# Kernel optimization log

Hardware: AMD Instinct MI355X
Metric: run time of the kernel (lower is better)

Reference implementation:

```python
import jax, jax.numpy as jnp
import numpy as np

INF = 1000000000.0
D = 1024


def setup_inputs() -> dict:
    key = jax.random.key(0)
    k_enc, k_r = jax.random.split(key)
    encoding = jax.random.normal(k_enc, (8, 2048, D), dtype=jnp.float32)
    R = jax.random.normal(k_r, (D, D), dtype=jnp.float32) / D  # init_with_zeros=False
    return {"encoding": encoding, "R": R}


def reference(encoding, R):
    b, n, d = encoding.shape
    # Q = encoding @ R ; scores = Q @ encoding^T  (bilinear relation attention)
    encR = jnp.einsum("bnd,de->bne", encoding, R)          # [b, n, d]
    scores = jnp.einsum("bnd,bmd->bnm", encR, encoding)     # [b, n, n]
    # causal mask: -INF above the diagonal (use_mask=True)
    mask = jnp.where(jnp.tril(jnp.ones((n, n), dtype=bool)), 0.0, -INF).astype(scores.dtype)
    A = jax.nn.softmax(scores + mask, axis=2)               # [b, n, n]
    return jnp.einsum("bnm,bmd->bnd", A, encoding)          # [b, n, d]
```

## Files before the change

kernel.cpp:

```cpp
#include <hip/hip_runtime.h>
#include <hip/hip_bf16.h>


typedef __attribute__((ext_vector_type(4))) float f32x4;
typedef __attribute__((ext_vector_type(4))) unsigned u32x4;
typedef __attribute__((ext_vector_type(8))) __fp16 f16x8;
typedef __attribute__((ext_vector_type(4))) __fp16 f16x4;
typedef __attribute__((ext_vector_type(2))) __fp16 f16x2;

#define MFMA16H(A, B, C) __builtin_amdgcn_mfma_f32_16x16x32_f16(A, B, C, 0, 0, 0)

__device__ __forceinline__ f16x4 cvt4h(f32x4 a) {
    union { f16x4 v; f16x2 h[2]; } r;
    r.h[0] = __builtin_amdgcn_cvt_pkrtz(a[0], a[1]);
    r.h[1] = __builtin_amdgcn_cvt_pkrtz(a[2], a[3]);
    return r.v;
}

__device__ __forceinline__ void gload16(const void* g, void* l) {
    __builtin_amdgcn_global_load_lds(
        (const __attribute__((address_space(1))) unsigned*)g,
        (__attribute__((address_space(3))) unsigned*)l, 16, 0, 0);
}

#define BAR() do { __builtin_amdgcn_sched_barrier(0); \
                   __builtin_amdgcn_s_barrier();      \
                   __builtin_amdgcn_sched_barrier(0); } while (0)

__global__ __launch_bounds__(256) void transpose_cvt_kernel(
    const float* __restrict__ enc, __fp16* __restrict__ encT, __fp16* __restrict__ encH,
    const float* __restrict__ R, __fp16* __restrict__ Rt)
{
    __shared__ __align__(16) char lt[64 * 128];
    const int t = threadIdx.x;
    const int bz = blockIdx.z;
    const bool isR = (bz == 8);
    if (isR && blockIdx.x >= 16) return;
    const int Rr = isR ? 1024 : 2048, C = 1024;
    const float* src = isR ? R : enc;
    __fp16* dstT = isR ? Rt : encT;
    __fp16* dstH = isR ? (__fp16*)nullptr : encH;
    const int r0 = blockIdx.x * 64, c0 = blockIdx.y * 64;
    const size_t so = isR ? 0 : (size_t)bz * Rr * C;
    const int tr = t >> 4;
    const int tc4 = (t & 15) * 4;
#pragma unroll
    for (int p = 0; p < 4; ++p) {
        int rl = tr + 16 * p;
        f32x4 x = *(const f32x4*)(src + so + (size_t)(r0 + rl) * C + c0 + tc4);
        f16x4 h = cvt4h(x);
        if (dstH) *(f16x4*)(dstH + so + (size_t)(r0 + rl) * C + c0 + tc4) = h;
        *(f16x4*)(lt + rl * 128 + ((tc4 * 2) ^ ((rl & 7) << 4))) = h;
    }
    __syncthreads();
#pragma unroll
    for (int p = 0; p < 4; ++p) {
        int dl = tr + 16 * p;
#pragma unroll
        for (int j = 0; j < 4; ++j) {
            int kl = (t & 15) + 16 * j;
            __fp16 v = *(const __fp16*)(lt + kl * 128 + ((dl * 2) ^ ((kl & 7) << 4)));
            dstT[so + (size_t)(c0 + dl) * Rr + r0 + kl] = v;
        }
    }
}

__global__ __launch_bounds__(512, 2) void gemm_qr256(
    const __fp16* __restrict__ encH, const __fp16* __restrict__ Rt,
    __fp16* __restrict__ Qh)
{
    __shared__ __align__(16) char lds[131072];
    const int t = threadIdx.x;
    const int w = t >> 6, l = t & 63;
    const int l15 = l & 15, lg = (l >> 4) & 3;
    const int wr = w >> 2, wc = w & 3;
    const int bm = ((int)blockIdx.x >> 2) * 256;
    const int bn = ((int)blockIdx.x & 3) * 256;
    const __fp16* Ag = encH + (size_t)bm * 1024;
    const __fp16* Bg = Rt + (size_t)bn * 1024;

    const int srow = 32 * w + (l >> 2);
    const int slg = ((l & 3) - ((l >> 3) & 3)) & 3;
    const int slotr = ((l >> 4) + ((l & 15) >> 1)) & 3;

    f32x4 acc[8][4];
#pragma unroll
    for (int i = 0; i < 8; ++i)
#pragma unroll
        for (int j = 0; j < 4; ++j) acc[i][j] = (f32x4){0.f, 0.f, 0.f, 0.f};

    auto stage = [&](int op, int tile, int kh) {
        const __fp16* src = (op ? Bg : Ag) + (size_t)srow * 1024 + tile * 64 + kh * 32 + slg * 8;
        char* dst = lds + (tile & 1) * 65536 + op * 32768 + kh * 16384 + w * 2048;
        gload16(src, dst);
        gload16(src + (size_t)16 * 1024, dst + 1024);
    };
    auto rdA = [&](int buf, int ks, int mf) {
        return *(const f16x8*)(lds + buf * 65536 + ks * 16384
                               + (128 * wr + 16 * mf + l15) * 64 + slotr * 16);
    };
    auto rdB = [&](int buf, int ks, int nf) {
        return *(const f16x8*)(lds + buf * 65536 + 32768 + ks * 16384
                               + (64 * wc + 16 * nf + l15) * 64 + slotr * 16);
    };

    stage(0, 0, 0); stage(1, 0, 0); stage(0, 0, 1); stage(1, 0, 1);
    stage(0, 1, 0); stage(1, 1, 0);

    f16x8 afr[4], bfr[4];

#define MF16(mbase)                                                     \
    __builtin_amdgcn_s_setprio(1);                                      \
    _Pragma("unroll") for (int mf = 0; mf < 4; ++mf)                    \
        _Pragma("unroll") for (int nf = 0; nf < 4; ++nf)                \
            acc[(mbase) + mf][nf] = MFMA16H(afr[mf], bfr[nf], acc[(mbase) + mf][nf]); \
    __builtin_amdgcn_s_setprio(0);

    for (int i = 0; i < 8; ++i) {
        const bool lastI = (i == 7);
        asm volatile("s_waitcnt vmcnt(8)" ::: "memory");
        BAR();
#pragma unroll
        for (int nf = 0; nf < 4; ++nf) bfr[nf] = rdB(0, 0, nf);
#pragma unroll
        for (int mf = 0; mf < 4; ++mf) afr[mf] = rdA(0, 0, mf);
        stage(0, 2 * i + 1, 1);
        MF16(0)
        BAR();
#pragma unroll
        for (int mf = 0; mf < 4; ++mf) afr[mf] = rdA(0, 0, mf + 4);
        stage(1, 2 * i + 1, 1);
        MF16(4)
        asm volatile("s_waitcnt vmcnt(8)" ::: "memory");
        BAR();
#pragma unroll
        for (int nf = 0; nf < 4; ++nf) bfr[nf] = rdB(0, 1, nf);
#pragma unroll
        for (int mf = 0; mf < 4; ++mf) afr[mf] = rdA(0, 1, mf);
        if (!lastI) stage(0, 2 * i + 2, 0);
        MF16(0)
        BAR();
#pragma unroll
        for (int mf = 0; mf < 4; ++mf) afr[mf] = rdA(0, 1, mf + 4);
        if (!lastI) stage(1, 2 * i + 2, 0);
        MF16(4)
        if (!lastI) asm volatile("s_waitcnt vmcnt(8)" ::: "memory");
        else        asm volatile("s_waitcnt vmcnt(4)" ::: "memory");
        BAR();
#pragma unroll
        for (int nf = 0; nf < 4; ++nf) bfr[nf] = rdB(1, 0, nf);
#pragma unroll
        for (int mf = 0; mf < 4; ++mf) afr[mf] = rdA(1, 0, mf);
        if (!lastI) stage(0, 2 * i + 2, 1);
        MF16(0)
        BAR();
#pragma unroll
        for (int mf = 0; mf < 4; ++mf) afr[mf] = rdA(1, 0, mf + 4);
        if (!lastI) stage(1, 2 * i + 2, 1);
        MF16(4)
        if (!lastI) asm volatile("s_waitcnt vmcnt(8)" ::: "memory");
        else        asm volatile("s_waitcnt vmcnt(0)" ::: "memory");
        BAR();
#pragma unroll
        for (int nf = 0; nf < 4; ++nf) bfr[nf] = rdB(1, 1, nf);
#pragma unroll
        for (int mf = 0; mf < 4; ++mf) afr[mf] = rdA(1, 1, mf);
        if (!lastI) stage(0, 2 * i + 3, 0);
        MF16(0)
        BAR();
#pragma unroll
        for (int mf = 0; mf < 4; ++mf) afr[mf] = rdA(1, 1, mf + 4);
        if (!lastI) stage(1, 2 * i + 3, 0);
        MF16(4)
    }
#undef MF16

#pragma unroll
    for (int mf = 0; mf < 8; ++mf)
#pragma unroll
        for (int nf = 0; nf < 4; ++nf)
#pragma unroll
            for (int rg = 0; rg < 4; ++rg) {
                int rr = bm + 128 * wr + 16 * mf + 4 * lg + rg;
                int cc = bn + 64 * wc + 16 * nf + l15;
                Qh[(size_t)rr * 1024 + cc] = (__fp16)acc[mf][nf][rg];
            }
}

template <int CMODE>
__device__ __forceinline__ void core256x128(
    const __fp16* __restrict__ A, int ldA, const __fp16* __restrict__ B, int ldB,
    char* __restrict__ Cptr, int ldC, int K, int rowOff, int colOff, bool maskDiag)
{
    __shared__ __align__(16) char lds[73728];
    const int t = threadIdx.x;
    const int w = t >> 6, l = t & 63;
    const int l15 = l & 15, lg = (l >> 4) & 3;
    const int wr = w >> 1, wc = w & 1;

    const int srowA = 32 * w + (l >> 2);
    const int srowB = 16 * w + (l >> 2);
    const int slg = ((l & 3) - ((l >> 3) & 3)) & 3;
    const int slotr = ((l >> 4) + ((l & 15) >> 1)) & 3;

    f32x4 acc[4][4];
#pragma unroll
    for (int i = 0; i < 4; ++i)
#pragma unroll
        for (int j = 0; j < 4; ++j) acc[i][j] = (f32x4){0.f, 0.f, 0.f, 0.f};

    auto stageH = [&](int h) {
        const int reg = h % 3;
        const __fp16* sa = A + (size_t)srowA * ldA + h * 32 + slg * 8;
        char* da = lds + reg * 16384 + w * 2048;
        gload16(sa, da);
        gload16(sa + (size_t)16 * ldA, da + 1024);
        const __fp16* sb = B + (size_t)srowB * ldB + h * 32 + slg * 8;
        gload16(sb, lds + 49152 + reg * 8192 + w * 1024);
    };
    auto rdA = [&](int h, int mf) {
        return *(const f16x8*)(lds + (h % 3) * 16384
                               + (64 * wr + 16 * mf + l15) * 64 + slotr * 16);
    };
    auto rdB = [&](int h, int nf) {
        return *(const f16x8*)(lds + 49152 + (h % 3) * 8192
                               + (64 * wc + 16 * nf + l15) * 64 + slotr * 16);
    };

    const int nh = K >> 5;
    stageH(0); stageH(1);

    f16x8 afr[4], bfr[4];
    for (int h = 0; h < nh; ++h) {
        if (h + 1 < nh) asm volatile("s_waitcnt vmcnt(3)" ::: "memory");
        else            asm volatile("s_waitcnt vmcnt(0)" ::: "memory");
        BAR();
#pragma unroll
        for (int nf = 0; nf < 4; ++nf) bfr[nf] = rdB(h, nf);
#pragma unroll
        for (int mf = 0; mf < 4; ++mf) afr[mf] = rdA(h, mf);
        if (h + 2 < nh) stageH(h + 2);
        __builtin_amdgcn_s_setprio(1);
#pragma unroll
        for (int mf = 0; mf < 4; ++mf)
#pragma unroll
            for (int nf = 0; nf < 4; ++nf)
                acc[mf][nf] = MFMA16H(afr[mf], bfr[nf], acc[mf][nf]);
        __builtin_amdgcn_s_setprio(0);
    }
    BAR();

#pragma unroll
    for (int mf = 0; mf < 4; ++mf)
#pragma unroll
        for (int nf = 0; nf < 4; ++nf)
#pragma unroll
            for (int rg = 0; rg < 4; ++rg) {
                int rr = 64 * wr + 16 * mf + 4 * lg + rg;
                int cc = 64 * wc + 16 * nf + l15;
                float v = acc[mf][nf][rg];
                if (CMODE == 2) {
                    *(float*)(Cptr + ((size_t)rr * ldC + cc) * 4) = v;
                } else {
                    if (maskDiag && colOff + cc > rowOff + rr) v = -30000.f;
                    *(__fp16*)(Cptr + ((size_t)rr * ldC + cc) * 2) = (__fp16)v;
                }
            }
}

__global__ __launch_bounds__(512, 4) void gemm_s256(
    const __fp16* __restrict__ Qh, const __fp16* __restrict__ encH,
    __fp16* __restrict__ S)
{
    const int b = (int)blockIdx.x & 7;
    const int r = (int)blockIdx.x >> 3;
    int qt = 0;
    while (r >= (qt + 1) * (qt + 2)) ++qt;
    const int nt = r - qt * (qt + 1);
    const size_t bo = (size_t)b * 2048 * 1024;
    const size_t so = (size_t)b * 2048 * 2048;
    core256x128<1>(Qh + bo + (size_t)(256 * qt) * 1024, 1024,
                   encH + bo + (size_t)(128 * nt) * 1024, 1024,
                   (char*)(S + so + (size_t)(256 * qt) * 2048 + 128 * nt), 2048,
                   1024, 256 * qt, 128 * nt, (nt >> 1) == qt);
}

__global__ __launch_bounds__(512, 4) void gemm_pv256(
    const __fp16* __restrict__ P, const __fp16* __restrict__ encT,
    float* __restrict__ out)
{
    const int b = (int)blockIdx.x & 7;
    const int r = (int)blockIdx.x >> 3;
    const int qtb = 7 - (r >> 3);
    const int dblk = r & 7;
    const size_t so = (size_t)b * 2048 * 2048;
    const size_t to = (size_t)b * 1024 * 2048;
    const size_t oo = (size_t)b * 2048 * 1024;
    core256x128<2>(P + so + (size_t)(256 * qtb) * 2048, 2048,
                   encT + to + (size_t)(128 * dblk) * 2048, 2048,
                   (char*)(out + oo + (size_t)(256 * qtb) * 1024 + 128 * dblk), 1024,
                   256 * (qtb + 1), 0, 0, false);
}

__global__ __launch_bounds__(256) void softmax_kernel(__fp16* __restrict__ S, int sh)
{
    const int t = threadIdx.x;
    const int wv = t >> 6, l = t & 63;
    const int r = blockIdx.x * 4 + wv;
    const int b = blockIdx.y;
    __fp16* row = S + ((size_t)b * 2048 + r) * 2048;
    const int L = ((r >> sh) + 1) << sh;

    float v[4][8];
    float mx = -1e30f;
#pragma unroll
    for (int i = 0; i < 4; ++i) {
        int c0 = 8 * l + 512 * i;
        if (c0 < L) {
            f16x8 h = *reinterpret_cast<const f16x8*>(row + c0);
#pragma unroll
            for (int j = 0; j < 8; ++j) { v[i][j] = (float)h[j]; mx = fmaxf(mx, v[i][j]); }
        } else {
#pragma unroll
            for (int j = 0; j < 8; ++j) v[i][j] = -1e30f;
        }
    }
#pragma unroll
    for (int off = 1; off < 64; off <<= 1) mx = fmaxf(mx, __shfl_xor(mx, off));
    float sm = 0.f;
#pragma unroll
    for (int i = 0; i < 4; ++i)
#pragma unroll
        for (int j = 0; j < 8; ++j) { v[i][j] = __expf(v[i][j] - mx); sm += v[i][j]; }
#pragma unroll
    for (int off = 1; off < 64; off <<= 1) sm += __shfl_xor(sm, off);
    const float inv = 1.f / sm;
#pragma unroll
    for (int i = 0; i < 4; ++i) {
        int c0 = 8 * l + 512 * i;
        if (c0 < L) {
            union { f16x8 v8; f16x2 h[4]; } o;
#pragma unroll
            for (int j = 0; j < 4; ++j)
                o.h[j] = __builtin_amdgcn_cvt_pkrtz(v[i][2 * j] * inv, v[i][2 * j + 1] * inv);
            *reinterpret_cast<f16x8*>(row + c0) = o.v8;
        }
    }
}

__global__ __launch_bounds__(256) void qr_gemm_kernel(
    const float* __restrict__ A, const float* __restrict__ B, float* C)
{
    __shared__ __align__(16) char sA[128 * 64];
    __shared__ __align__(16) char sB[128 * 64];
    const int t = threadIdx.x;
    const int w = t >> 6, l = t & 63;
    const int l15 = l & 15, lg = l >> 4;
    const int bm = blockIdx.x * 128;
    const int bn = blockIdx.y * 128;

    f32x4 acc[4][4];
#pragma unroll
    for (int i = 0; i < 4; ++i)
#pragma unroll
        for (int j = 0; j < 4; ++j) acc[i][j] = (f32x4){0.f, 0.f, 0.f, 0.f};

    const int kq = 4 * (t & 7);
    const int i2 = t >> 3;

    for (int kk = 0; kk < 1024; kk += 32) {
#pragma unroll
        for (int it = 0; it < 4; ++it) {
            int m = i2 + 32 * it;
            f32x4 x = *reinterpret_cast<const f32x4*>(&A[(size_t)(bm + m) * 1024 + kk + kq]);
            *reinterpret_cast<f16x4*>(sA + m * 64 + ((2 * kq) ^ (((m >> 1) & 3) << 4))) = cvt4h(x);
        }
        {
            int n0 = 4 * i2;
            f32x4 x[4];
#pragma unroll
            for (int r = 0; r < 4; ++r)
                x[r] = *reinterpret_cast<const f32x4*>(&B[(size_t)(kk + kq + r) * 1024 + bn + n0]);
#pragma unroll
            for (int j = 0; j < 4; ++j) {
                int n = n0 + j;
                union { f16x4 v; f16x2 h[2]; } s;
                s.h[0] = __builtin_amdgcn_cvt_pkrtz(x[0][j], x[1][j]);
                s.h[1] = __builtin_amdgcn_cvt_pkrtz(x[2][j], x[3][j]);
                *reinterpret_cast<f16x4*>(sB + n * 64 + ((2 * kq) ^ (((n >> 1) & 3) << 4))) = s.v;
            }
        }
        __syncthreads();
        f16x8 af[4], bfv[4];
        const int r0 = (w >> 1) * 64, c0 = (w & 1) * 64;
#pragma unroll
        for (int mt = 0; mt < 4; ++mt) {
            int m = r0 + 16 * mt + l15;
            af[mt] = *reinterpret_cast<f16x8*>(sA + m * 64 + ((16 * lg) ^ (((m >> 1) & 3) << 4)));
        }
#pragma unroll
        for (int nt = 0; nt < 4; ++nt) {
            int n = c0 + 16 * nt + l15;
            bfv[nt] = *reinterpret_cast<f16x8*>(sB + n * 64 + ((16 * lg) ^ (((n >> 1) & 3) << 4)));
        }
#pragma unroll
        for (int mt = 0; mt < 4; ++mt)
#pragma unroll
            for (int nt = 0; nt < 4; ++nt)
                acc[mt][nt] = MFMA16H(af[mt], bfv[nt], acc[mt][nt]);
        __syncthreads();
    }
#pragma unroll
    for (int mt = 0; mt < 4; ++mt)
#pragma unroll
        for (int nt = 0; nt < 4; ++nt)
#pragma unroll
            for (int rg = 0; rg < 4; ++rg) {
                int row = bm + (w >> 1) * 64 + 16 * mt + 4 * lg + rg;
                int col = bn + (w & 1) * 64 + 16 * nt + l15;
                C[(size_t)row * 1024 + col] = acc[mt][nt][rg];
            }
}

__global__ __launch_bounds__(256) void s_gemm_kernel(
    const float* __restrict__ Q, const float* __restrict__ enc, __fp16* __restrict__ S)
{
    __shared__ __align__(16) char sA[128 * 64];
    __shared__ __align__(16) char sB[128 * 64];
    const int t = threadIdx.x;
    const int w = t >> 6, l = t & 63;
    const int l15 = l & 15, lg = l >> 4;

    int rem = 135 - (int)blockIdx.x;
    int qt = 0;
    while (rem > qt) { rem -= qt + 1; ++qt; }
    const int kt = rem;
    const int b = blockIdx.y;
    const float* Arow = Q + ((size_t)b * 2048 + qt * 128) * 1024;
    const float* Brow = enc + ((size_t)b * 2048 + kt * 128) * 1024;

    f32x4 acc[4][4];
#pragma unroll
    for (int i = 0; i < 4; ++i)
#pragma unroll
        for (int j = 0; j < 4; ++j) acc[i][j] = (f32x4){0.f, 0.f, 0.f, 0.f};

    const int kq = 4 * (t & 7);
    const int i2 = t >> 3;

    for (int kk = 0; kk < 1024; kk += 32) {
#pragma unroll
        for (int it = 0; it < 4; ++it) {
            int m = i2 + 32 * it;
            int sw = (2 * kq) ^ (((m >> 1) & 3) << 4);
            f32x4 xa = *reinterpret_cast<const f32x4*>(&Arow[(size_t)m * 1024 + kk + kq]);
            f32x4 xb = *reinterpret_cast<const f32x4*>(&Brow[(size_t)m * 1024 + kk + kq]);
            *reinterpret_cast<f16x4*>(sA + m * 64 + sw) = cvt4h(xa);
            *reinterpret_cast<f16x4*>(sB + m * 64 + sw) = cvt4h(xb);
        }
        __syncthreads();
        f16x8 af[4], bfv[4];
        const int r0 = (w >> 1) * 64, c0 = (w & 1) * 64;
#pragma unroll
        for (int mt = 0; mt < 4; ++mt) {
            int m = r0 + 16 * mt + l15;
            af[mt] = *reinterpret_cast<f16x8*>(sA + m * 64 + ((16 * lg) ^ (((m >> 1) & 3) << 4)));
        }
#pragma unroll
        for (int nt = 0; nt < 4; ++nt) {
            int n = c0 + 16 * nt + l15;
            bfv[nt] = *reinterpret_cast<f16x8*>(sB + n * 64 + ((16 * lg) ^ (((n >> 1) & 3) << 4)));
        }
#pragma unroll
        for (int mt = 0; mt < 4; ++mt)
#pragma unroll
            for (int nt = 0; nt < 4; ++nt)
                acc[mt][nt] = MFMA16H(af[mt], bfv[nt], acc[mt][nt]);
        __syncthreads();
    }
    const int r0 = (w >> 1) * 64, c0 = (w & 1) * 64;
#pragma unroll
    for (int mt = 0; mt < 4; ++mt)
#pragma unroll
        for (int nt = 0; nt < 4; ++nt)
#pragma unroll
            for (int rg = 0; rg < 4; ++rg) {
                int rt = r0 + 16 * mt + 4 * lg + rg;
                int ct = c0 + 16 * nt + l15;
                float v = acc[mt][nt][rg];
                if (kt == qt && ct > rt) v = -30000.f;
                S[((size_t)b * 2048 + qt * 128 + rt) * 2048 + kt * 128 + ct] = (__fp16)v;
            }
}

__global__ __launch_bounds__(512) void pv_gemm_kernel(
    const __fp16* __restrict__ P, const float* __restrict__ enc, float* __restrict__ out)
{
    __shared__ __align__(16) char sA[128 * 128];
    __shared__ __align__(16) char sB[128 * 128];
    const int t = threadIdx.x;
    const int w = t >> 6, l = t & 63;
    const int l15 = l & 15, lg = (l >> 4) & 3;
    const int wq = w >> 2, wdv = w & 3;
    const int qtb = 15 - (int)blockIdx.x;
    const int dblk = blockIdx.y;
    const int b = blockIdx.z;
    const int q0 = 128 * qtb;
    const int nkv = 128 * (qtb + 1);
    const __fp16* Pbase = P + ((size_t)b * 2048 + q0) * 2048;
    const float* Eb = enc + (size_t)b * 2048 * 1024;

    f32x4 acc[4][2];
#pragma unroll
    for (int i = 0; i < 4; ++i)
#pragma unroll
        for (int j = 0; j < 2; ++j) acc[i][j] = (f32x4){0.f, 0.f, 0.f, 0.f};

    const int ar = t >> 2, aseg = t & 3;
    const int ba = t >> 5, bdq = t & 31;

    for (int kv0 = 0; kv0 < nkv; kv0 += 64) {
        __syncthreads();
        {
            const __fp16* src = Pbase + (size_t)ar * 2048 + kv0 + 16 * aseg;
            u32x4 v0 = *reinterpret_cast<const u32x4*>(src);
            u32x4 v1 = *reinterpret_cast<const u32x4*>(src + 8);
            const int sw = (ar & 7) << 4;
            *reinterpret_cast<u32x4*>(sA + ar * 128 + ((32 * aseg) ^ sw)) = v0;
            *reinterpret_cast<u32x4*>(sA + ar * 128 + ((32 * aseg + 16) ^ sw)) = v1;
        }
        {
            const float* src = Eb + (size_t)(kv0 + 4 * ba) * 1024 + 128 * dblk + 4 * bdq;
            f32x4 x0 = *reinterpret_cast<const f32x4*>(src);
            f32x4 x1 = *reinterpret_cast<const f32x4*>(src + 1024);
            f32x4 x2 = *reinterpret_cast<const f32x4*>(src + 2048);
            f32x4 x3 = *reinterpret_cast<const f32x4*>(src + 3072);
#pragma unroll
            for (int j = 0; j < 4; ++j) {
                int d = 4 * bdq + j;
                union { f16x4 v; f16x2 h[2]; } s;
                s.h[0] = __builtin_amdgcn_cvt_pkrtz(x0[j], x1[j]);
                s.h[1] = __builtin_amdgcn_cvt_pkrtz(x2[j], x3[j]);
                *reinterpret_cast<f16x4*>(sB + d * 128 + ((8 * ba) ^ ((d & 7) << 4))) = s.v;
            }
        }
        __syncthreads();
#pragma unroll
        for (int ks = 0; ks < 2; ++ks) {
            f16x8 afr[4], bfr[2];
#pragma unroll
            for (int mt = 0; mt < 4; ++mt) {
                int rr = 64 * wq + 16 * mt + l15;
                afr[mt] = *reinterpret_cast<f16x8*>(sA + rr * 128 + ((64 * ks + 16 * lg) ^ ((rr & 7) << 4)));
            }
#pragma unroll
            for (int nt = 0; nt < 2; ++nt) {
                int d = 32 * wdv + 16 * nt + l15;
                bfr[nt] = *reinterpret_cast<f16x8*>(sB + d * 128 + ((64 * ks + 16 * lg) ^ ((d & 7) << 4)));
            }
#pragma unroll
            for (int mt = 0; mt < 4; ++mt)
#pragma unroll
                for (int nt = 0; nt < 2; ++nt)
                    acc[mt][nt] = MFMA16H(afr[mt], bfr[nt], acc[mt][nt]);
        }
    }
#pragma unroll
    for (int mt = 0; mt < 4; ++mt)
#pragma unroll
        for (int nt = 0; nt < 2; ++nt)
#pragma unroll
            for (int rg = 0; rg < 4; ++rg) {
                size_t row = (size_t)b * 2048 + q0 + 64 * wq + 16 * mt + 4 * lg + rg;
                int col = 128 * dblk + 32 * wdv + 16 * nt + l15;
                out[row * 1024 + col] = acc[mt][nt][rg];
            }
}

extern "C" void kernel_launch(void* const* d_in, const int* in_sizes, int n_in,
                              void* d_out, int out_size, void* d_ws, size_t ws_size,
                              hipStream_t stream)
{
    const float* enc = (const float*)d_in[0];
    const float* R = (const float*)d_in[1];
    float* out = (float*)d_out;
    const size_t MB = 1u << 20;

    if (ws_size >= 98 * MB) {
        __fp16* S = (__fp16*)d_ws;
        __fp16* encT = (__fp16*)((char*)d_ws + 64 * MB);
        __fp16* Rt = (__fp16*)((char*)d_ws + 96 * MB);
        __fp16* Qh = (__fp16*)d_out;
        __fp16* encH = (__fp16*)d_out + (size_t)16384 * 1024;

        transpose_cvt_kernel<<<dim3(32, 16, 9), 256, 0, stream>>>(enc, encT, encH, R, Rt);
        gemm_qr256<<<dim3(256), 512, 0, stream>>>(encH, Rt, Qh);
        gemm_s256<<<dim3(576), 512, 0, stream>>>(Qh, encH, S);
        softmax_kernel<<<dim3(512, 8), 256, 0, stream>>>(S, 8);
        gemm_pv256<<<dim3(512), 512, 0, stream>>>(S, encT, out);
    } else {
        __fp16* S = (__fp16*)d_ws;
        qr_gemm_kernel<<<dim3(128, 8), 256, 0, stream>>>(enc, R, out);
        s_gemm_kernel<<<dim3(136, 8), 256, 0, stream>>>(out, enc, S);
        softmax_kernel<<<dim3(512, 8), 256, 0, stream>>>(S, 7);
        pv_gemm_kernel<<<dim3(16, 8, 8), 512, 0, stream>>>(S, enc, out);
    }
}
```

Measured before the change: 181.5 us.

## Fuse softmax exp and row sums into score GEMM epilogue, normalize in PV

The score GEMM epilogue now writes exp(score) in fp16, with masked entries set to zero, and accumulates per-row sums into a global buffer via shuffle reductions and atomics. The PV GEMM multiplies its output by the reciprocal row sum, so the separate softmax kernel and its read/write pass over S are skipped. It skips max subtraction, which depends on scores staying small enough that exp does not overflow fp16. It also adds a memset and atomic traffic. The path is enabled only when the workspace is large enough to hold the row-sum buffer.

```diff
diff --git a/kernel.cpp b/kernel.cpp
--- a/kernel.cpp
+++ b/kernel.cpp
@@ -190,7 +190,8 @@
 template <int CMODE>
 __device__ __forceinline__ void core256x128(
     const __fp16* __restrict__ A, int ldA, const __fp16* __restrict__ B, int ldB,
-    char* __restrict__ Cptr, int ldC, int K, int rowOff, int colOff, bool maskDiag)
+    char* __restrict__ Cptr, int ldC, int K, int rowOff, int colOff, bool maskDiag,
+    float* __restrict__ Lsum, int lrowBase)
 {
     __shared__ __align__(16) char lds[73728];
     const int t = threadIdx.x;
@@ -250,27 +251,68 @@
     }
     BAR();
 
-#pragma unroll
-    for (int mf = 0; mf < 4; ++mf)
-#pragma unroll
-        for (int nf = 0; nf < 4; ++nf)
-#pragma unroll
-            for (int rg = 0; rg < 4; ++rg) {
-                int rr = 64 * wr + 16 * mf + 4 * lg + rg;
-                int cc = 64 * wc + 16 * nf + l15;
-                float v = acc[mf][nf][rg];
-                if (CMODE == 2) {
-                    *(float*)(Cptr + ((size_t)rr * ldC + cc) * 4) = v;
-                } else {
-                    if (maskDiag && colOff + cc > rowOff + rr) v = -30000.f;
-                    *(__fp16*)(Cptr + ((size_t)rr * ldC + cc) * 2) = (__fp16)v;
+    if (CMODE == 1) {
+        float rsum[4][4];
+#pragma unroll
+        for (int mf = 0; mf < 4; ++mf)
+#pragma unroll
+            for (int rg = 0; rg < 4; ++rg) rsum[mf][rg] = 0.f;
+#pragma unroll
+        for (int mf = 0; mf < 4; ++mf)
+#pragma unroll
+            for (int nf = 0; nf < 4; ++nf)
+#pragma unroll
+                for (int rg = 0; rg < 4; ++rg) {
+                    int rr = 64 * wr + 16 * mf + 4 * lg + rg;
+                    int cc = 64 * wc + 16 * nf + l15;
+                    float v = acc[mf][nf][rg];
+                    bool msk = maskDiag && (colOff + cc > rowOff + rr);
+                    if (Lsum) {
+                        float e = msk ? 0.f : __expf(v);
+                        rsum[mf][rg] += e;
+                        *(__fp16*)(Cptr + ((size_t)rr * ldC + cc) * 2) = (__fp16)e;
+                    } else {
+                        if (msk) v = -30000.f;
+                        *(__fp16*)(Cptr + ((size_t)rr * ldC + cc) * 2) = (__fp16)v;
+                    }
                 }
-            }
+        if (Lsum) {
+#pragma unroll
+            for (int mf = 0; mf < 4; ++mf)
+#pragma unroll
+                for (int rg = 0; rg < 4; ++rg) {
+                    float s = rsum[mf][rg];
+                    s += __shfl_xor(s, 1);
+                    s += __shfl_xor(s, 2);
+                    s += __shfl_xor(s, 4);
+                    s += __shfl_xor(s, 8);
+                    if (l15 == 0)
+                        atomicAdd(&Lsum[lrowBase + 64 * wr + 16 * mf + 4 * lg + rg], s);
+                }
+        }
+    } else {
+        float scl[4][4];
+#pragma unroll
+        for (int mf = 0; mf < 4; ++mf)
+#pragma unroll
+            for (int rg = 0; rg < 4; ++rg)
+                scl[mf][rg] = Lsum ? (1.f / Lsum[lrowBase + 64 * wr + 16 * mf + 4 * lg + rg]) : 1.f;
+#pragma unroll
+        for (int mf = 0; mf < 4; ++mf)
+#pragma unroll
+            for (int nf = 0; nf < 4; ++nf)
+#pragma unroll
+                for (int rg = 0; rg < 4; ++rg) {
+                    int rr = 64 * wr + 16 * mf + 4 * lg + rg;
+                    int cc = 64 * wc + 16 * nf + l15;
+                    *(float*)(Cptr + ((size_t)rr * ldC + cc) * 4) = acc[mf][nf][rg] * scl[mf][rg];
+                }
+    }
 }
 
 __global__ __launch_bounds__(512, 4) void gemm_s256(
     const __fp16* __restrict__ Qh, const __fp16* __restrict__ encH,
-    __fp16* __restrict__ S)
+    __fp16* __restrict__ S, float* __restrict__ Lsum)
 {
     const int b = (int)blockIdx.x & 7;
     const int r = (int)blockIdx.x >> 3;
@@ -282,12 +324,13 @@
     core256x128<1>(Qh + bo + (size_t)(256 * qt) * 1024, 1024,
                    encH + bo + (size_t)(128 * nt) * 1024, 1024,
                    (char*)(S + so + (size_t)(256 * qt) * 2048 + 128 * nt), 2048,
-                   1024, 256 * qt, 128 * nt, (nt >> 1) == qt);
+                   1024, 256 * qt, 128 * nt, (nt >> 1) == qt,
+                   Lsum, b * 2048 + 256 * qt);
 }
 
 __global__ __launch_bounds__(512, 4) void gemm_pv256(
     const __fp16* __restrict__ P, const __fp16* __restrict__ encT,
-    float* __restrict__ out)
+    float* __restrict__ out, float* __restrict__ Lsum)
 {
     const int b = (int)blockIdx.x & 7;
     const int r = (int)blockIdx.x >> 3;
@@ -299,7 +342,8 @@
     core256x128<2>(P + so + (size_t)(256 * qtb) * 2048, 2048,
                    encT + to + (size_t)(128 * dblk) * 2048, 2048,
                    (char*)(out + oo + (size_t)(256 * qtb) * 1024 + 128 * dblk), 1024,
-                   256 * (qtb + 1), 0, 0, false);
+                   256 * (qtb + 1), 0, 0, false,
+                   Lsum, b * 2048 + 256 * qtb);
 }
 
 __global__ __launch_bounds__(256) void softmax_kernel(__fp16* __restrict__ S, int sh)
@@ -592,12 +636,15 @@
         __fp16* Rt = (__fp16*)((char*)d_ws + 96 * MB);
         __fp16* Qh = (__fp16*)d_out;
         __fp16* encH = (__fp16*)d_out + (size_t)16384 * 1024;
+        const bool fused = ws_size >= 98 * MB + 65536;
+        float* Lsum = fused ? (float*)((char*)d_ws + 98 * MB) : nullptr;
 
         transpose_cvt_kernel<<<dim3(32, 16, 9), 256, 0, stream>>>(enc, encT, encH, R, Rt);
         gemm_qr256<<<dim3(256), 512, 0, stream>>>(encH, Rt, Qh);
-        gemm_s256<<<dim3(576), 512, 0, stream>>>(Qh, encH, S);
-        softmax_kernel<<<dim3(512, 8), 256, 0, stream>>>(S, 8);
-        gemm_pv256<<<dim3(512), 512, 0, stream>>>(S, encT, out);
+        if (fused) hipMemsetAsync(Lsum, 0, 65536, stream);
+        gemm_s256<<<dim3(576), 512, 0, stream>>>(Qh, encH, S, Lsum);
+        if (!fused) softmax_kernel<<<dim3(512, 8), 256, 0, stream>>>(S, 8);
+        gemm_pv256<<<dim3(512), 512, 0, stream>>>(S, encT, out, Lsum);
     } else {
         __fp16* S = (__fp16*)d_ws;
         qr_gemm_kernel<<<dim3(128, 8), 256, 0, stream>>>(enc, R, out);
```

After: 175.6 us. 3.2% less time.
